# Kernel optimization log

Hardware: AMD Instinct MI355X
Metric: run time of the kernel (lower is better)

The kernel has to match this reference:

```python
import jax, jax.numpy as jnp
import numpy as np

B, S, A = 65536, 376, 17
H1, H2, K = 400, 300, 15
MAX_ACTION = 1.0


def setup_inputs() -> dict:
    key = jax.random.key(0)
    ks = jax.random.split(key, 16)

    def lin(kw, fan_in, fan_out):
        lim = 1.0 / np.sqrt(fan_in)
        k1, k2 = jax.random.split(kw)
        W = jax.random.uniform(k1, (fan_in, fan_out), jnp.float32, -lim, lim)
        b = jax.random.uniform(k2, (fan_out,), jnp.float32, -lim, lim)
        return W, b

    W1, b1 = lin(ks[0], S, H1)
    W2, b2 = lin(ks[1], H1, H2)
    Wmu, bmu = lin(ks[2], H2, A)
    Wlv, blv = lin(ks[3], H2, A)
    Wu, bu = lin(ks[4], H2, K * A)
    Ww, bw = lin(ks[5], H2, K * A)
    Wb, bb = lin(ks[6], H2, K)
    x = jax.random.normal(ks[7], (B, S), jnp.float32)
    eps = jax.random.normal(ks[8], (B, A), jnp.float32)
    return dict(x=x, eps=eps, W1=W1, b1=b1, W2=W2, b2=b2, Wmu=Wmu, bmu=bmu,
                Wlv=Wlv, blv=blv, Wu=Wu, bu=bu, Ww=Ww, bw=bw, Wb=Wb, bb=bb)


def _flow_chain(action, u, w, b):
    # u, w: (K, B, A); b: (K, B). Sequential planar flow -> lax.scan over K.
    def step(carry, uwb):
        z, ldj = carry
        u_k, w_k, b_k = uwb
        uw = jnp.sum(w_k * u_k, -1)                       # (B,)
        m_uw = -1.0 + jax.nn.softplus(uw)
        w_norm_sq = jnp.sum(w_k * w_k, -1)
        u_hat = u_k + ((m_uw - uw) / w_norm_sq)[:, None] * w_k  # invertibility reparam
        wzb = jnp.sum(w_k * z, -1) + b_k                  # (B,)
        t = jnp.tanh(wzb)
        z_new = z + u_hat * t[:, None]
        psi_u = jnp.sum(w_k * u_hat, -1) * (1.0 - t * t)  # psi^T u_hat
        ldj_new = ldj + jnp.log(jnp.abs(1.0 + psi_u))
        return (z_new, ldj_new), None

    init = (action, jnp.zeros(action.shape[0], action.dtype))
    (z_fin, ldj), _ = jax.lax.scan(step, init, (u, w, b))
    return z_fin, ldj


def reference(x, eps, W1, b1, W2, b2, Wmu, bmu, Wlv, blv, Wu, bu, Ww, bw, Wb, bb):
    h = jax.nn.relu(x @ W1 + b1)
    h = jax.nn.relu(h @ W2 + b2)
    mu = MAX_ACTION * jnp.tanh(h @ Wmu + bmu)
    log_var = MAX_ACTION * jnp.tanh(h @ Wlv + blv)
    std = jnp.exp(log_var)                 # torch code uses log_var.exp() as the scale
    action = mu + std * eps                # rsample

    u = (h @ Wu + bu).reshape(B, K, A).transpose(1, 0, 2)   # (K, B, A)
    w = (h @ Ww + bw).reshape(B, K, A).transpose(1, 0, 2)   # (K, B, A)
    b = (h @ Wb + bb).T                                      # (K, B)

    final_action, log_det_j = _flow_chain(action, u, w, b)

    # Normal(mu, std).log_prob(action) summed over action dim; (action-mu)/std == eps
    log_2pi = jnp.float32(np.log(2.0 * np.pi))
    log_prob = jnp.sum(-0.5 * eps * eps - log_var - 0.5 * log_2pi, axis=-1)
    log_prob_final = log_prob - log_det_j
    prob_final = jnp.exp(log_prob_final)
    return final_action, prob_final, log_prob_final
```

## Files before the change

kernel.cpp:

```cpp
#include <hip/hip_runtime.h>

typedef unsigned short ushort_t;
typedef unsigned int uint_t;
typedef __bf16 bf16x8 __attribute__((ext_vector_type(8)));
typedef float f32x4 __attribute__((ext_vector_type(4)));

#define B_ROWS 65536

#define KT1 12
#define NT1 30
#define KTC1 15
#define KI2 13
#define NT2 20
#define KTC2 10
#define KI3 10
#define NT3 50
#define KTH 25


#define SZ1 (NT1 * KT1 * 512)
#define SZ2 (NT2 * KI2 * 512)
#define SZ3 (NT3 * KI3 * 512)

#define H2_US    ((size_t)4096 * KTC2 * 512)
#define HEADS_US ((size_t)4096 * KTH * 512)

__device__ inline ushort_t f2bf(float f) {
    uint_t u = __float_as_uint(f);
    return (ushort_t)((u + 0x7FFFu + ((u >> 16) & 1u)) >> 16);
}
__device__ inline uint_t pack2(float a, float b) {
    return (uint_t)f2bf(a) | ((uint_t)f2bf(b) << 16);
}
__device__ inline float fast_tanh(float x) {
    float e = __expf(2.f * x);
    return 1.f - 2.f / (e + 1.f);
}
__device__ inline void gl2lds16(const ushort_t* g, ushort_t* l) {
    __builtin_amdgcn_global_load_lds(
        (const __attribute__((address_space(1))) uint_t*)g,
        (__attribute__((address_space(3))) uint_t*)l, 16, 0, 0);
}
__device__ inline void unpack8(uint4 v, float* dst) {
    uint_t q[4] = {v.x, v.y, v.z, v.w};
    #pragma unroll
    for (int m = 0; m < 4; ++m) {
        dst[2 * m]     = __uint_as_float(q[m] << 16);
        dst[2 * m + 1] = __uint_as_float(q[m] & 0xFFFF0000u);
    }
}

__global__ void pack_kernel(const float* __restrict__ W1, const float* __restrict__ W2,
                            const float* __restrict__ Wmu, const float* __restrict__ Wlv,
                            const float* __restrict__ Wu, const float* __restrict__ Ww,
                            const float* __restrict__ Wb,
                            const float* __restrict__ b1, const float* __restrict__ b2,
                            const float* __restrict__ bmu, const float* __restrict__ blv,
                            const float* __restrict__ bu, const float* __restrict__ bw,
                            const float* __restrict__ bb,
                            ushort_t* __restrict__ W1t, ushort_t* __restrict__ W2t,
                            ushort_t* __restrict__ Wht,
                            float* __restrict__ b1p, float* __restrict__ b2p,
                            float* __restrict__ bHp)
{
    int i = blockIdx.x * 256 + threadIdx.x;
    if (i < SZ1) {
        int t = i >> 9, pos = i & 511;
        int l = pos >> 3, j = pos & 7;
        int n = (t / KT1) * 16 + (l & 15);
        int k = (t % KT1) * 32 + (l >> 4) * 8 + j;
        W1t[i] = (n < 400 && k < 376) ? f2bf(W1[k * 400 + n]) : (ushort_t)0;
    } else if (i < SZ1 + SZ2) {
        int i2 = i - SZ1;
        int t = i2 >> 9, pos = i2 & 511;
        int l = pos >> 3, j = pos & 7;
        int n = (t / KI2) * 16 + (l & 15);
        int k = (t % KI2) * 32 + (l >> 4) * 8 + j;
        W2t[i2] = (n < 300 && k < 400) ? f2bf(W2[k * 300 + n]) : (ushort_t)0;
    } else if (i < SZ1 + SZ2 + SZ3) {
        int i3 = i - SZ1 - SZ2;
        int t = i3 >> 9, pos = i3 & 511;
        int l = pos >> 3, j = pos & 7;
        int n = (t / KI3) * 16 + (l & 15);
        int k = (t % KI3) * 32 + (l >> 4) * 8 + j;
        float v = 0.f;
        if (k < 300) {
            if (n < 24)      { if (n < 17) v = Wmu[k * 17 + n]; }
            else if (n < 48) { int c = n - 24; if (c < 17) v = Wlv[k * 17 + c]; }
            else if (n < 64) { int c = n - 48; if (c < 15) v = Wb[k * 15 + c]; }
            else if (n < 784) {
                int r = n - 64, slot = r / 48, c = r % 48;
                if (c < 24) { if (c < 17) v = Wu[k * 255 + slot * 17 + c]; }
                else        { int c2 = c - 24; if (c2 < 17) v = Ww[k * 255 + slot * 17 + c2]; }
            }
        }
        Wht[i3] = f2bf(v);
    } else {
        int j = i - SZ1 - SZ2 - SZ3;
        if (j < 480) {
            b1p[j] = (j < 400) ? b1[j] : 0.f;
        } else if (j < 800) {
            int n = j - 480;
            b2p[n] = (n < 300) ? b2[n] : 0.f;
        } else if (j < 1600) {
            int n = j - 800;
            float v = 0.f;
            if (n < 24)      { if (n < 17) v = bmu[n]; }
            else if (n < 48) { int c = n - 24; if (c < 17) v = blv[c]; }
            else if (n < 64) { int c = n - 48; if (c < 15) v = bb[c]; }
            else if (n < 784) {
                int r = n - 64, slot = r / 48, c = r % 48;
                if (c < 24) { if (c < 17) v = bu[slot * 17 + c]; }
                else        { int c2 = c - 24; if (c2 < 17) v = bw[slot * 17 + c2]; }
            }
            bHp[n] = v;
        }
    }
}

template<int KITERS, int NX, bool RELU, bool CVT_A>
__global__ __launch_bounds__(512, 4)
void gemm_rs(const ushort_t* __restrict__ At, const float* __restrict__ xf,
             const ushort_t* __restrict__ Bt, const float* __restrict__ bias,
             ushort_t* __restrict__ C, int kTA, int kTC)
{
    __shared__ ushort_t Bs[2][10 * 512];
    const int tid = threadIdx.x;
    const int lane = tid & 63, wv = tid >> 6;
    const int wr = wv >> 1, wc = wv & 1;
    const int q = lane >> 4, l16 = lane & 15;

    const int b = blockIdx.x;
    const int xcd = b & 7, idx = b >> 3;
    const int grp = idx / NX;
    const int bx = idx - grp * NX;
    const int by = xcd + grp * 8;
    const int nb0 = bx * 10;
    const int rowblk0 = by * 8;

    f32x4 acc[2][5];
    #pragma unroll
    for (int r = 0; r < 2; ++r)
        #pragma unroll
        for (int c = 0; c < 5; ++c)
            acc[r][c] = (f32x4){0.f, 0.f, 0.f, 0.f};

    auto loadA = [&](int kt, bf16x8* a) {
        #pragma unroll
        for (int r = 0; r < 2; ++r) {
            int rt = rowblk0 + wr * 2 + r;
            if (CVT_A) {
                int row = rt * 16 + l16;
                int k0 = kt * 32 + q * 8;
                uint4 o = {0u, 0u, 0u, 0u};
                if (k0 + 8 <= 376) {
                    const float4* p = reinterpret_cast<const float4*>(
                        xf + (size_t)row * 376 + k0);
                    float4 v0 = p[0], v1 = p[1];
                    o.x = pack2(v0.x, v0.y); o.y = pack2(v0.z, v0.w);
                    o.z = pack2(v1.x, v1.y); o.w = pack2(v1.z, v1.w);
                }
                a[r] = __builtin_bit_cast(bf16x8, o);
            } else {
                a[r] = __builtin_bit_cast(bf16x8, *reinterpret_cast<const uint4*>(
                    At + (((size_t)rt * kTA + kt) << 9) + lane * 8));
            }
        }
    };
    auto stageB = [&](int kt, int buf) {
        gl2lds16(Bt + (((size_t)(nb0 + wv) * KITERS + kt) << 9) + lane * 8,
                 &Bs[buf][wv << 9]);
        if (wv < 2)
            gl2lds16(Bt + (((size_t)(nb0 + 8 + wv) * KITERS + kt) << 9) + lane * 8,
                     &Bs[buf][(8 + wv) << 9]);
    };

    stageB(0, 0);
    bf16x8 ac[2];
    loadA(0, ac);
    __syncthreads();

    #pragma unroll
    for (int kt = 0; kt < KITERS; ++kt) {
        const int p = kt & 1;
        bf16x8 an[2];
        if (kt + 1 < KITERS) {
            stageB(kt + 1, p ^ 1);
            loadA(kt + 1, an);
        }
        #pragma unroll
        for (int c = 0; c < 5; ++c) {
            bf16x8 bb = __builtin_bit_cast(bf16x8, *reinterpret_cast<const uint4*>(
                &Bs[p][((wc * 5 + c) << 9) + lane * 8]));
            acc[0][c] = __builtin_amdgcn_mfma_f32_16x16x32_bf16(ac[0], bb, acc[0][c], 0, 0, 0);
            acc[1][c] = __builtin_amdgcn_mfma_f32_16x16x32_bf16(ac[1], bb, acc[1][c], 0, 0, 0);
        }
        __syncthreads();
        if (kt + 1 < KITERS) { ac[0] = an[0]; ac[1] = an[1]; }
    }

    #pragma unroll
    for (int r = 0; r < 2; ++r) {
        int rowblk = rowblk0 + wr * 2 + r;
        #pragma unroll
        for (int c = 0; c < 5; ++c) {
            int n = (nb0 + wc * 5 + c) * 16 + l16;
            float bv = bias[n];
            #pragma unroll
            for (int reg = 0; reg < 4; ++reg) {
                float v = acc[r][c][reg] + bv;
                if (RELU) v = fmaxf(v, 0.f);
                int mrow = q * 4 + reg;
                size_t off = (((size_t)rowblk * kTC + (n >> 5)) << 9)
                           + (size_t)(((n >> 3) & 3) * 16 + mrow) * 8 + (n & 7);
                C[off] = f2bf(v);
            }
        }
    }
}

__device__ inline void ld_group8(const ushort_t* hb, int g, float* dst) {
    uint4 v = *reinterpret_cast<const uint4*>(hb + ((g >> 2) << 9) + ((g & 3) << 7));
    unpack8(v, dst);
}

__global__ __launch_bounds__(256, 4)
void flow_kernel(const ushort_t* __restrict__ heads, const float* __restrict__ eps,
                 float* __restrict__ out, int Btot)
{
    const int tid = threadIdx.x;
    const int sub = tid & 3;
    const long row = (long)blockIdx.x * 64 + (tid >> 2);
    const ushort_t* hb = heads + (((size_t)(row >> 4) * KTH) << 9)
                               + (size_t)((row & 15) << 3);

    float z[8];
    float lp = 0.f;
    {
        float amu[8] = {0,0,0,0,0,0,0,0}, alv[8] = {0,0,0,0,0,0,0,0};
        if (sub < 3) {
            ld_group8(hb, sub, amu);
            ld_group8(hb, 3 + sub, alv);
        }
        float ep[8];
        #pragma unroll
        for (int c = 0; c < 8; ++c) {
            int i = sub * 8 + c;
            ep[c] = (i < 17) ? eps[row * 17 + i] : 0.f;
        }
        #pragma unroll
        for (int c = 0; c < 8; ++c) {
            float mu = fast_tanh(amu[c]);
            float lv = fast_tanh(alv[c]);
            z[c] = mu + __expf(lv) * ep[c];
            int i = sub * 8 + c;
            lp += (i < 17) ? (-0.5f * ep[c] * ep[c] - lv - 0.918938533f) : 0.f;
        }
    }

    float bv[16];
    ld_group8(hb, 6, &bv[0]);
    ld_group8(hb, 7, &bv[8]);

    float ldj = 0.f;
    #pragma unroll
    for (int k = 0; k < 15; ++k) {
        float au[8] = {0,0,0,0,0,0,0,0}, aw[8] = {0,0,0,0,0,0,0,0};
        if (sub < 3) {
            ld_group8(hb, 8 + 6 * k + sub, au);
            ld_group8(hb, 11 + 6 * k + sub, aw);
        }
        float uw = 0.f, w2 = 0.f, wz = 0.f;
        #pragma unroll
        for (int c = 0; c < 8; ++c) {
            uw += aw[c] * au[c];
            w2 += aw[c] * aw[c];
            wz += aw[c] * z[c];
        }
        uw += __shfl_xor(uw, 1); uw += __shfl_xor(uw, 2);
        w2 += __shfl_xor(w2, 1); w2 += __shfl_xor(w2, 2);
        wz += __shfl_xor(wz, 1); wz += __shfl_xor(wz, 2);

        float sp = (uw > 15.f) ? uw : __logf(1.f + __expf(uw));
        float m = sp - 1.f;
        float coef = (m - uw) / fmaxf(w2, 1e-20f);
        float t = fast_tanh(wz + bv[k]);
        #pragma unroll
        for (int c = 0; c < 8; ++c)
            z[c] += (au[c] + coef * aw[c]) * t;
        float psi = m * (1.f - t * t);
        ldj += __logf(fmaxf(fabsf(1.f + psi), 1e-30f));
    }

    lp += __shfl_xor(lp, 1); lp += __shfl_xor(lp, 2);
    #pragma unroll
    for (int c = 0; c < 8; ++c) {
        int i = sub * 8 + c;
        if (i < 17) out[row * 17 + i] = z[c];
    }
    float lpf = lp - ldj;
    if (sub == 0) {
        out[(long)Btot * 17 + row] = __expf(lpf);
        out[(long)Btot * 18 + row] = lpf;
    }
}

extern "C" void kernel_launch(void* const* d_in, const int* in_sizes, int n_in,
                              void* d_out, int out_size, void* d_ws, size_t ws_size,
                              hipStream_t stream)
{
    const float* x   = (const float*)d_in[0];
    const float* eps = (const float*)d_in[1];
    float* out = (float*)d_out;

    ushort_t* ws = (ushort_t*)d_ws;
    ushort_t* R_h2    = ws;
    ushort_t* R_h1    = ws + H2_US;
    ushort_t* R_heads = ws + H2_US;
    ushort_t* W1t = ws + H2_US + HEADS_US;
    ushort_t* W2t = W1t + SZ1;
    ushort_t* Wht = W2t + SZ2;
    float* b1p = (float*)(Wht + SZ3);
    float* b2p = b1p + 480;
    float* bHp = b2p + 320;

    const int packN = SZ1 + SZ2 + SZ3 + 1600;
    pack_kernel<<<(packN + 255) / 256, 256, 0, stream>>>(
        (const float*)d_in[2],  (const float*)d_in[4],
        (const float*)d_in[6],  (const float*)d_in[8],
        (const float*)d_in[10], (const float*)d_in[12], (const float*)d_in[14],
        (const float*)d_in[3],  (const float*)d_in[5],
        (const float*)d_in[7],  (const float*)d_in[9],
        (const float*)d_in[11], (const float*)d_in[13], (const float*)d_in[15],
        W1t, W2t, Wht, b1p, b2p, bHp);

    gemm_rs<KT1, 3, true, true><<<3 * 512, 512, 0, stream>>>(
        nullptr, x, W1t, b1p, R_h1, 0, KTC1);
    gemm_rs<KI2, 2, true, false><<<2 * 512, 512, 0, stream>>>(
        R_h1, nullptr, W2t, b2p, R_h2, KTC1, KTC2);
    gemm_rs<KI3, 5, false, false><<<5 * 512, 512, 0, stream>>>(
        R_h2, nullptr, Wht, bHp, R_heads, KTC2, KTH);
    flow_kernel<<<B_ROWS / 64, 256, 0, stream>>>(R_heads, eps, out, B_ROWS);
}
```

Baseline: 350.8 us.

## Preload full weight panel into LDS and prefetch A registers several k-steps ahead

The GEMM kernel now stages the block's entire B weight panel (all k-tiles) into LDS at the start, in place of double-buffering one k-tile per iteration. The per-iteration __syncthreads is removed. A fragments are issued P=4 k-steps ahead into register arrays; for the first layer the raw fp32 values are buffered and converted to bf16 at use. This is meant to cut barrier stalls and hide global load latency. In exchange it uses far more LDS (up to 130KB for the 13-k-tile layer) and more registers, so launch bounds drop to 2 blocks per CU and occupancy may fall.

```diff
diff --git a/kernel.cpp b/kernel.cpp
--- a/kernel.cpp
+++ b/kernel.cpp
@@ -119,12 +119,12 @@
 }
 
 template<int KITERS, int NX, bool RELU, bool CVT_A>
-__global__ __launch_bounds__(512, 4)
-void gemm_rs(const ushort_t* __restrict__ At, const float* __restrict__ xf,
+__global__ __launch_bounds__(512, 2)
+void gemm_bp(const ushort_t* __restrict__ At, const float* __restrict__ xf,
              const ushort_t* __restrict__ Bt, const float* __restrict__ bias,
              ushort_t* __restrict__ C, int kTA, int kTC)
 {
-    __shared__ ushort_t Bs[2][10 * 512];
+    __shared__ ushort_t Bs[KITERS * 10 * 512];
     const int tid = threadIdx.x;
     const int lane = tid & 63, wv = tid >> 6;
     const int wr = wv >> 1, wc = wv & 1;
@@ -138,65 +138,73 @@
     const int nb0 = bx * 10;
     const int rowblk0 = by * 8;
 
-    f32x4 acc[2][5];
-    #pragma unroll
-    for (int r = 0; r < 2; ++r)
-        #pragma unroll
-        for (int c = 0; c < 5; ++c)
-            acc[r][c] = (f32x4){0.f, 0.f, 0.f, 0.f};
-
-    auto loadA = [&](int kt, bf16x8* a) {
+    for (int t = wv; t < KITERS * 10; t += 8) {
+        int n = t / KITERS, kt = t - n * KITERS;
+        gl2lds16(Bt + (((size_t)nb0 * KITERS + t) << 9) + lane * 8,
+                 &Bs[(kt * 10 + n) << 9]);
+    }
+
+    constexpr int P = (KITERS < 4) ? KITERS : 4;
+    float4 rawA[CVT_A ? KITERS : 1][4];
+    uint4  binA[CVT_A ? 1 : KITERS][2];
+
+    auto issueA = [&](int kt) {
         #pragma unroll
         for (int r = 0; r < 2; ++r) {
             int rt = rowblk0 + wr * 2 + r;
             if (CVT_A) {
                 int row = rt * 16 + l16;
                 int k0 = kt * 32 + q * 8;
-                uint4 o = {0u, 0u, 0u, 0u};
+                float4 lo = {0.f, 0.f, 0.f, 0.f}, hi = {0.f, 0.f, 0.f, 0.f};
                 if (k0 + 8 <= 376) {
                     const float4* p = reinterpret_cast<const float4*>(
                         xf + (size_t)row * 376 + k0);
-                    float4 v0 = p[0], v1 = p[1];
-                    o.x = pack2(v0.x, v0.y); o.y = pack2(v0.z, v0.w);
-                    o.z = pack2(v1.x, v1.y); o.w = pack2(v1.z, v1.w);
+                    lo = p[0]; hi = p[1];
                 }
+                rawA[CVT_A ? kt : 0][2 * r] = lo;
+                rawA[CVT_A ? kt : 0][2 * r + 1] = hi;
+            } else {
+                binA[CVT_A ? 0 : kt][r] = *reinterpret_cast<const uint4*>(
+                    At + (((size_t)rt * kTA + kt) << 9) + lane * 8);
+            }
+        }
+    };
+
+    f32x4 acc[2][5];
+    #pragma unroll
+    for (int r = 0; r < 2; ++r)
+        #pragma unroll
+        for (int c = 0; c < 5; ++c)
+            acc[r][c] = (f32x4){0.f, 0.f, 0.f, 0.f};
+
+    #pragma unroll
+    for (int i = 0; i < P; ++i) issueA(i);
+    __syncthreads();
+
+    #pragma unroll
+    for (int kt = 0; kt < KITERS; ++kt) {
+        bf16x8 a[2];
+        #pragma unroll
+        for (int r = 0; r < 2; ++r) {
+            if (CVT_A) {
+                float4 lo = rawA[CVT_A ? kt : 0][2 * r];
+                float4 hi = rawA[CVT_A ? kt : 0][2 * r + 1];
+                uint4 o;
+                o.x = pack2(lo.x, lo.y); o.y = pack2(lo.z, lo.w);
+                o.z = pack2(hi.x, hi.y); o.w = pack2(hi.z, hi.w);
                 a[r] = __builtin_bit_cast(bf16x8, o);
             } else {
-                a[r] = __builtin_bit_cast(bf16x8, *reinterpret_cast<const uint4*>(
-                    At + (((size_t)rt * kTA + kt) << 9) + lane * 8));
-            }
-        }
-    };
-    auto stageB = [&](int kt, int buf) {
-        gl2lds16(Bt + (((size_t)(nb0 + wv) * KITERS + kt) << 9) + lane * 8,
-                 &Bs[buf][wv << 9]);
-        if (wv < 2)
-            gl2lds16(Bt + (((size_t)(nb0 + 8 + wv) * KITERS + kt) << 9) + lane * 8,
-                     &Bs[buf][(8 + wv) << 9]);
-    };
-
-    stageB(0, 0);
-    bf16x8 ac[2];
-    loadA(0, ac);
-    __syncthreads();
-
-    #pragma unroll
-    for (int kt = 0; kt < KITERS; ++kt) {
-        const int p = kt & 1;
-        bf16x8 an[2];
-        if (kt + 1 < KITERS) {
-            stageB(kt + 1, p ^ 1);
-            loadA(kt + 1, an);
-        }
+                a[r] = __builtin_bit_cast(bf16x8, binA[CVT_A ? 0 : kt][r]);
+            }
+        }
+        if (kt + P < KITERS) issueA(kt + P);
         #pragma unroll
         for (int c = 0; c < 5; ++c) {
             bf16x8 bb = __builtin_bit_cast(bf16x8, *reinterpret_cast<const uint4*>(
-                &Bs[p][((wc * 5 + c) << 9) + lane * 8]));
-            acc[0][c] = __builtin_amdgcn_mfma_f32_16x16x32_bf16(ac[0], bb, acc[0][c], 0, 0, 0);
-            acc[1][c] = __builtin_amdgcn_mfma_f32_16x16x32_bf16(ac[1], bb, acc[1][c], 0, 0, 0);
-        }
-        __syncthreads();
-        if (kt + 1 < KITERS) { ac[0] = an[0]; ac[1] = an[1]; }
+                &Bs[((kt * 10 + wc * 5 + c) << 9) + lane * 8]));
+            acc[0][c] = __builtin_amdgcn_mfma_f32_16x16x32_bf16(a[0], bb, acc[0][c], 0, 0, 0);
+            acc[1][c] = __builtin_amdgcn_mfma_f32_16x16x32_bf16(a[1], bb, acc[1][c], 0, 0, 0);
+        }
     }
 
     #pragma unroll
@@ -334,11 +342,11 @@
         (const float*)d_in[11], (const float*)d_in[13], (const float*)d_in[15],
         W1t, W2t, Wht, b1p, b2p, bHp);
 
-    gemm_rs<KT1, 3, true, true><<<3 * 512, 512, 0, stream>>>(
+    gemm_bp<KT1, 3, true, true><<<3 * 512, 512, 0, stream>>>(
         nullptr, x, W1t, b1p, R_h1, 0, KTC1);
-    gemm_rs<KI2, 2, true, false><<<2 * 512, 512, 0, stream>>>(
+    gemm_bp<KI2, 2, true, false><<<2 * 512, 512, 0, stream>>>(
         R_h1, nullptr, W2t, b2p, R_h2, KTC1, KTC2);
-    gemm_rs<KI3, 5, false, false><<<5 * 512, 512, 0, stream>>>(
+    gemm_bp<KI3, 5, false, false><<<5 * 512, 512, 0, stream>>>(
         R_h2, nullptr, Wht, bHp, R_heads, KTC2, KTH);
     flow_kernel<<<B_ROWS / 64, 256, 0, stream>>>(R_heads, eps, out, B_ROWS);
 }
```

New measurement: 346.8 us. About the same (-1.1%).

## Fuse heads GEMM into flow kernel via LDS and drop LDS staging in GEMMs

Applied to the files above, without the earlier changes.

The heads GEMM and the planar-flow kernel are merged into one kernel. Each block computes its 64 rows of head outputs into shared memory, then runs the flow chain from LDS, which removes the global round trip of the heads tensor. The remaining GEMMs drop the LDS double-buffered B staging and instead load B fragments straight from global into registers, using 256-thread blocks with 4x5 tiles per wave. Risks include more register pressure, 100 KB of LDS per fused block limiting occupancy, half the threads sitting idle in the flow phase, and redundant B reads from global.

```diff
diff --git a/kernel.cpp b/kernel.cpp
--- a/kernel.cpp
+++ b/kernel.cpp
@@ -14,7 +14,7 @@
 #define NT2 20
 #define KTC2 10
 #define KI3 10
-#define NT3 50
+#define NT3 52
 #define KTH 25
 
 
@@ -22,8 +22,8 @@
 #define SZ2 (NT2 * KI2 * 512)
 #define SZ3 (NT3 * KI3 * 512)
 
-#define H2_US    ((size_t)4096 * KTC2 * 512)
-#define HEADS_US ((size_t)4096 * KTH * 512)
+#define H2_US ((size_t)4096 * KTC2 * 512)
+#define H1_US ((size_t)4096 * KTC1 * 512)
 
 __device__ inline ushort_t f2bf(float f) {
     uint_t u = __float_as_uint(f);
@@ -35,11 +35,6 @@
 __device__ inline float fast_tanh(float x) {
     float e = __expf(2.f * x);
     return 1.f - 2.f / (e + 1.f);
-}
-__device__ inline void gl2lds16(const ushort_t* g, ushort_t* l) {
-    __builtin_amdgcn_global_load_lds(
-        (const __attribute__((address_space(1))) uint_t*)g,
-        (__attribute__((address_space(3))) uint_t*)l, 16, 0, 0);
 }
 __device__ inline void unpack8(uint4 v, float* dst) {
     uint_t q[4] = {v.x, v.y, v.z, v.w};
@@ -102,7 +97,7 @@
         } else if (j < 800) {
             int n = j - 480;
             b2p[n] = (n < 300) ? b2[n] : 0.f;
-        } else if (j < 1600) {
+        } else if (j < 1632) {
             int n = j - 800;
             float v = 0.f;
             if (n < 24)      { if (n < 17) v = bmu[n]; }
@@ -119,15 +114,14 @@
 }
 
 template<int KITERS, int NX, bool RELU, bool CVT_A>
-__global__ __launch_bounds__(512, 4)
-void gemm_rs(const ushort_t* __restrict__ At, const float* __restrict__ xf,
+__global__ __launch_bounds__(256, 4)
+void gemm_nb(const ushort_t* __restrict__ At, const float* __restrict__ xf,
              const ushort_t* __restrict__ Bt, const float* __restrict__ bias,
              ushort_t* __restrict__ C, int kTA, int kTC)
 {
-    __shared__ ushort_t Bs[2][10 * 512];
     const int tid = threadIdx.x;
     const int lane = tid & 63, wv = tid >> 6;
-    const int wr = wv >> 1, wc = wv & 1;
+    const int mh = wv >> 1, nh = wv & 1;
     const int q = lane >> 4, l16 = lane & 15;
 
     const int b = blockIdx.x;
@@ -138,17 +132,19 @@
     const int nb0 = bx * 10;
     const int rowblk0 = by * 8;
 
-    f32x4 acc[2][5];
-    #pragma unroll
-    for (int r = 0; r < 2; ++r)
+    f32x4 acc[4][5];
+    #pragma unroll
+    for (int r = 0; r < 4; ++r)
         #pragma unroll
         for (int c = 0; c < 5; ++c)
             acc[r][c] = (f32x4){0.f, 0.f, 0.f, 0.f};
 
-    auto loadA = [&](int kt, bf16x8* a) {
-        #pragma unroll
-        for (int r = 0; r < 2; ++r) {
-            int rt = rowblk0 + wr * 2 + r;
+    #pragma unroll
+    for (int kt = 0; kt < KITERS; ++kt) {
+        bf16x8 a[4];
+        #pragma unroll
+        for (int r = 0; r < 4; ++r) {
+            int rt = rowblk0 + mh * 4 + r;
             if (CVT_A) {
                 int row = rt * 16 + l16;
                 int k0 = kt * 32 + q * 8;
@@ -166,45 +162,25 @@
                     At + (((size_t)rt * kTA + kt) << 9) + lane * 8));
             }
         }
-    };
-    auto stageB = [&](int kt, int buf) {
-        gl2lds16(Bt + (((size_t)(nb0 + wv) * KITERS + kt) << 9) + lane * 8,
-                 &Bs[buf][wv << 9]);
-        if (wv < 2)
-            gl2lds16(Bt + (((size_t)(nb0 + 8 + wv) * KITERS + kt) << 9) + lane * 8,
-                     &Bs[buf][(8 + wv) << 9]);
-    };
-
-    stageB(0, 0);
-    bf16x8 ac[2];
-    loadA(0, ac);
-    __syncthreads();
-
-    #pragma unroll
-    for (int kt = 0; kt < KITERS; ++kt) {
-        const int p = kt & 1;
-        bf16x8 an[2];
-        if (kt + 1 < KITERS) {
-            stageB(kt + 1, p ^ 1);
-            loadA(kt + 1, an);
-        }
+        bf16x8 bfr[5];
+        #pragma unroll
+        for (int c = 0; c < 5; ++c)
+            bfr[c] = __builtin_bit_cast(bf16x8, *reinterpret_cast<const uint4*>(
+                Bt + (((size_t)(nb0 + nh * 5 + c) * KITERS + kt) << 9) + lane * 8));
+        #pragma unroll
+        for (int r = 0; r < 4; ++r)
+            #pragma unroll
+            for (int c = 0; c < 5; ++c)
+                acc[r][c] = __builtin_amdgcn_mfma_f32_16x16x32_bf16(
+                    a[r], bfr[c], acc[r][c], 0, 0, 0);
+    }
+
+    #pragma unroll
+    for (int r = 0; r < 4; ++r) {
+        int rowblk = rowblk0 + mh * 4 + r;
         #pragma unroll
         for (int c = 0; c < 5; ++c) {
-            bf16x8 bb = __builtin_bit_cast(bf16x8, *reinterpret_cast<const uint4*>(
-                &Bs[p][((wc * 5 + c) << 9) + lane * 8]));
-            acc[0][c] = __builtin_amdgcn_mfma_f32_16x16x32_bf16(ac[0], bb, acc[0][c], 0, 0, 0);
-            acc[1][c] = __builtin_amdgcn_mfma_f32_16x16x32_bf16(ac[1], bb, acc[1][c], 0, 0, 0);
-        }
-        __syncthreads();
-        if (kt + 1 < KITERS) { ac[0] = an[0]; ac[1] = an[1]; }
-    }
-
-    #pragma unroll
-    for (int r = 0; r < 2; ++r) {
-        int rowblk = rowblk0 + wr * 2 + r;
-        #pragma unroll
-        for (int c = 0; c < 5; ++c) {
-            int n = (nb0 + wc * 5 + c) * 16 + l16;
+            int n = (nb0 + nh * 5 + c) * 16 + l16;
             float bv = bias[n];
             #pragma unroll
             for (int reg = 0; reg < 4; ++reg) {
@@ -219,89 +195,144 @@
     }
 }
 
-__device__ inline void ld_group8(const ushort_t* hb, int g, float* dst) {
-    uint4 v = *reinterpret_cast<const uint4*>(hb + ((g >> 2) << 9) + ((g & 3) << 7));
-    unpack8(v, dst);
-}
-
-__global__ __launch_bounds__(256, 4)
-void flow_kernel(const ushort_t* __restrict__ heads, const float* __restrict__ eps,
-                 float* __restrict__ out, int Btot)
+__global__ __launch_bounds__(512, 2)
+void gemm_flow2(const ushort_t* __restrict__ At, const ushort_t* __restrict__ Bt,
+                const float* __restrict__ bias, const float* __restrict__ eps,
+                float* __restrict__ out)
 {
+    __shared__ ushort_t Hd[100 * 512];
     const int tid = threadIdx.x;
-    const int sub = tid & 3;
-    const long row = (long)blockIdx.x * 64 + (tid >> 2);
-    const ushort_t* hb = heads + (((size_t)(row >> 4) * KTH) << 9)
-                               + (size_t)((row & 15) << 3);
-
-    float z[8];
-    float lp = 0.f;
-    {
-        float amu[8] = {0,0,0,0,0,0,0,0}, alv[8] = {0,0,0,0,0,0,0,0};
-        if (sub < 3) {
-            ld_group8(hb, sub, amu);
-            ld_group8(hb, 3 + sub, alv);
-        }
-        float ep[8];
+    const int lane = tid & 63, wv = tid >> 6;
+    const int wm = wv >> 2, wn = wv & 3;
+    const int q = lane >> 4, l16 = lane & 15;
+    const long row0 = (long)blockIdx.x * 64;
+
+    f32x4 acc[2][13];
+    #pragma unroll
+    for (int r = 0; r < 2; ++r)
+        #pragma unroll
+        for (int c = 0; c < 13; ++c)
+            acc[r][c] = (f32x4){0.f, 0.f, 0.f, 0.f};
+
+    #pragma unroll
+    for (int kt = 0; kt < KI3; ++kt) {
+        bf16x8 a[2];
+        #pragma unroll
+        for (int r = 0; r < 2; ++r) {
+            size_t rtg = (size_t)blockIdx.x * 4 + wm * 2 + r;
+            a[r] = __builtin_bit_cast(bf16x8, *reinterpret_cast<const uint4*>(
+                At + ((rtg * KTC2 + kt) << 9) + lane * 8));
+        }
+        #pragma unroll
+        for (int c = 0; c < 13; ++c) {
+            bf16x8 bb = __builtin_bit_cast(bf16x8, *reinterpret_cast<const uint4*>(
+                Bt + (((size_t)(wn * 13 + c) * KI3 + kt) << 9) + lane * 8));
+            acc[0][c] = __builtin_amdgcn_mfma_f32_16x16x32_bf16(a[0], bb, acc[0][c], 0, 0, 0);
+            acc[1][c] = __builtin_amdgcn_mfma_f32_16x16x32_bf16(a[1], bb, acc[1][c], 0, 0, 0);
+        }
+    }
+
+    #pragma unroll
+    for (int r = 0; r < 2; ++r) {
+        int rts = wm * 2 + r;
+        #pragma unroll
+        for (int c = 0; c < 13; ++c) {
+            int nt = wn * 13 + c;
+            if (nt < 50) {
+                int n = nt * 16 + l16;
+                float bv = bias[n];
+                #pragma unroll
+                for (int reg = 0; reg < 4; ++reg) {
+                    int r16 = q * 4 + reg;
+                    Hd[((rts * KTH + (n >> 5)) << 9) + (((n >> 3) & 3) << 7)
+                       + (r16 << 3) + (n & 7)] = f2bf(acc[r][c][reg] + bv);
+                }
+            }
+        }
+    }
+    __syncthreads();
+
+    if (tid < 256) {
+        const int sub = tid & 3;
+        const int row = tid >> 2;
+        const ushort_t* hb = &Hd[(((row >> 4) * KTH) << 9) + ((row & 15) << 3)];
+        const long grow = row0 + row;
+
+        auto ldg8 = [&](int g, float* dst) {
+            uint4 v = *reinterpret_cast<const uint4*>(
+                hb + ((g >> 2) << 9) + ((g & 3) << 7));
+            unpack8(v, dst);
+        };
+
+        float z[8];
+        float lp = 0.f;
+        {
+            float amu[8] = {0,0,0,0,0,0,0,0}, alv[8] = {0,0,0,0,0,0,0,0};
+            if (sub < 3) {
+                ldg8(sub, amu);
+                ldg8(3 + sub, alv);
+            }
+            float ep[8];
+            #pragma unroll
+            for (int c = 0; c < 8; ++c) {
+                int i = sub * 8 + c;
+                ep[c] = (i < 17) ? eps[grow * 17 + i] : 0.f;
+            }
+            #pragma unroll
+            for (int c = 0; c < 8; ++c) {
+                float mu = fast_tanh(amu[c]);
+                float lv = fast_tanh(alv[c]);
+                z[c] = mu + __expf(lv) * ep[c];
+                int i = sub * 8 + c;
+                lp += (i < 17) ? (-0.5f * ep[c] * ep[c] - lv - 0.918938533f) : 0.f;
+            }
+        }
+
+        float bv[16];
+        ldg8(6, &bv[0]);
+        ldg8(7, &bv[8]);
+
+        float ldj = 0.f;
+        #pragma unroll
+        for (int k = 0; k < 15; ++k) {
+            float au[8] = {0,0,0,0,0,0,0,0}, aw[8] = {0,0,0,0,0,0,0,0};
+            if (sub < 3) {
+                ldg8(8 + 6 * k + sub, au);
+                ldg8(11 + 6 * k + sub, aw);
+            }
+            float uw = 0.f, w2 = 0.f, wz = 0.f;
+            #pragma unroll
+            for (int c = 0; c < 8; ++c) {
+                uw += aw[c] * au[c];
+                w2 += aw[c] * aw[c];
+                wz += aw[c] * z[c];
+            }
+            uw += __shfl_xor(uw, 1); uw += __shfl_xor(uw, 2);
+            w2 += __shfl_xor(w2, 1); w2 += __shfl_xor(w2, 2);
+            wz += __shfl_xor(wz, 1); wz += __shfl_xor(wz, 2);
+
+            float sp = (uw > 15.f) ? uw : __logf(1.f + __expf(uw));
+            float m = sp - 1.f;
+            float coef = (m - uw) / fmaxf(w2, 1e-20f);
+            float t = fast_tanh(wz + bv[k]);
+            #pragma unroll
+            for (int c = 0; c < 8; ++c)
+                z[c] += (au[c] + coef * aw[c]) * t;
+            float psi = m * (1.f - t * t);
+            ldj += __logf(fmaxf(fabsf(1.f + psi), 1e-30f));
+        }
+
+        lp += __shfl_xor(lp, 1); lp += __shfl_xor(lp, 2);
         #pragma unroll
         for (int c = 0; c < 8; ++c) {
             int i = sub * 8 + c;
-            ep[c] = (i < 17) ? eps[row * 17 + i] : 0.f;
-        }
-        #pragma unroll
-        for (int c = 0; c < 8; ++c) {
-            float mu = fast_tanh(amu[c]);
-            float lv = fast_tanh(alv[c]);
-            z[c] = mu + __expf(lv) * ep[c];
-            int i = sub * 8 + c;
-            lp += (i < 17) ? (-0.5f * ep[c] * ep[c] - lv - 0.918938533f) : 0.f;
-        }
-    }
-
-    float bv[16];
-    ld_group8(hb, 6, &bv[0]);
-    ld_group8(hb, 7, &bv[8]);
-
-    float ldj = 0.f;
-    #pragma unroll
-    for (int k = 0; k < 15; ++k) {
-        float au[8] = {0,0,0,0,0,0,0,0}, aw[8] = {0,0,0,0,0,0,0,0};
-        if (sub < 3) {
-            ld_group8(hb, 8 + 6 * k + sub, au);
-            ld_group8(hb, 11 + 6 * k + sub, aw);
-        }
-        float uw = 0.f, w2 = 0.f, wz = 0.f;
-        #pragma unroll
-        for (int c = 0; c < 8; ++c) {
-            uw += aw[c] * au[c];
-            w2 += aw[c] * aw[c];
-            wz += aw[c] * z[c];
-        }
-        uw += __shfl_xor(uw, 1); uw += __shfl_xor(uw, 2);
-        w2 += __shfl_xor(w2, 1); w2 += __shfl_xor(w2, 2);
-        wz += __shfl_xor(wz, 1); wz += __shfl_xor(wz, 2);
-
-        float sp = (uw > 15.f) ? uw : __logf(1.f + __expf(uw));
-        float m = sp - 1.f;
-        float coef = (m - uw) / fmaxf(w2, 1e-20f);
-        float t = fast_tanh(wz + bv[k]);
-        #pragma unroll
-        for (int c = 0; c < 8; ++c)
-            z[c] += (au[c] + coef * aw[c]) * t;
-        float psi = m * (1.f - t * t);
-        ldj += __logf(fmaxf(fabsf(1.f + psi), 1e-30f));
-    }
-
-    lp += __shfl_xor(lp, 1); lp += __shfl_xor(lp, 2);
-    #pragma unroll
-    for (int c = 0; c < 8; ++c) {
-        int i = sub * 8 + c;
-        if (i < 17) out[row * 17 + i] = z[c];
-    }
-    float lpf = lp - ldj;
-    if (sub == 0) {
-        out[(long)Btot * 17 + row] = __expf(lpf);
-        out[(long)Btot * 18 + row] = lpf;
+            if (i < 17) out[grow * 17 + i] = z[c];
+        }
+        float lpf = lp - ldj;
+        if (sub == 0) {
+            out[(long)B_ROWS * 17 + grow] = __expf(lpf);
+            out[(long)B_ROWS * 18 + grow] = lpf;
+        }
     }
 }
 
@@ -314,17 +345,16 @@
     float* out = (float*)d_out;
 
     ushort_t* ws = (ushort_t*)d_ws;
-    ushort_t* R_h2    = ws;
-    ushort_t* R_h1    = ws + H2_US;
-    ushort_t* R_heads = ws + H2_US;
-    ushort_t* W1t = ws + H2_US + HEADS_US;
+    ushort_t* R_h2 = ws;
+    ushort_t* R_h1 = ws + H2_US;
+    ushort_t* W1t = ws + H2_US + H1_US;
     ushort_t* W2t = W1t + SZ1;
     ushort_t* Wht = W2t + SZ2;
     float* b1p = (float*)(Wht + SZ3);
     float* b2p = b1p + 480;
     float* bHp = b2p + 320;
 
-    const int packN = SZ1 + SZ2 + SZ3 + 1600;
+    const int packN = SZ1 + SZ2 + SZ3 + 1632;
     pack_kernel<<<(packN + 255) / 256, 256, 0, stream>>>(
         (const float*)d_in[2],  (const float*)d_in[4],
         (const float*)d_in[6],  (const float*)d_in[8],
@@ -334,11 +364,9 @@
         (const float*)d_in[11], (const float*)d_in[13], (const float*)d_in[15],
         W1t, W2t, Wht, b1p, b2p, bHp);
 
-    gemm_rs<KT1, 3, true, true><<<3 * 512, 512, 0, stream>>>(
+    gemm_nb<KT1, 3, true, true><<<3 * 512, 256, 0, stream>>>(
         nullptr, x, W1t, b1p, R_h1, 0, KTC1);
-    gemm_rs<KI2, 2, true, false><<<2 * 512, 512, 0, stream>>>(
+    gemm_nb<KI2, 2, true, false><<<2 * 512, 256, 0, stream>>>(
         R_h1, nullptr, W2t, b2p, R_h2, KTC1, KTC2);
-    gemm_rs<KI3, 5, false, false><<<5 * 512, 512, 0, stream>>>(
-        R_h2, nullptr, Wht, bHp, R_heads, KTC2, KTH);
-    flow_kernel<<<B_ROWS / 64, 256, 0, stream>>>(R_heads, eps, out, B_ROWS);
-}
+    gemm_flow2<<<B_ROWS / 64, 512, 0, stream>>>(R_h2, Wht, bHp, eps, out);
+}
```

Measured after the change: 681.6 us. 94.3% more time.
